# Optimization experiments

Hardware: AMD Instinct MI355X
Metric: run time of the kernel (lower is better)

The kernel has to match this reference:

```python
import jax, jax.numpy as jnp
import numpy as np

HEADS = 8  # from init_kwargs

def setup_inputs() -> dict:
    key = jax.random.key(0)
    ks = jax.random.split(key, 9)
    N, S, E = 8, 2048, 512
    scale = 1.0 / np.sqrt(E)
    return {
        "values": jax.random.normal(ks[0], (N, S, E), jnp.float32),
        "keys": jax.random.normal(ks[1], (N, S, E), jnp.float32),
        "query": jax.random.normal(ks[2], (N, S, E), jnp.float32),
        "mask": jnp.ones((N, 1, 1, S), jnp.int32),
        "Wv": jax.random.normal(ks[3], (E, E), jnp.float32) * scale,
        "Wk": jax.random.normal(ks[4], (E, E), jnp.float32) * scale,
        "Wq": jax.random.normal(ks[5], (E, E), jnp.float32) * scale,
        "Wo": jax.random.normal(ks[6], (E, E), jnp.float32) * scale,
        "bo": jnp.zeros((E,), jnp.float32),
    }

def reference(values, keys, query, mask, Wv, Wk, Wq, Wo, bo):
    N, Q, E = query.shape
    H = HEADS
    D = E // H
    v = (values @ Wv).reshape(N, -1, H, D)  # [N,K,H,D]
    k = (keys @ Wk).reshape(N, -1, H, D)
    q = (query @ Wq).reshape(N, Q, H, D)
    energy = jnp.einsum('nqhd,nkhd->nhqk', q, k)  # [N,H,Q,K]
    energy = jnp.where(mask == 0, jnp.float32(-1e20), energy)
    attn = jax.nn.softmax(energy / jnp.sqrt(jnp.float32(D)), axis=3)
    out = jnp.einsum('nhqk,nkhd->nqhd', attn, v).reshape(N, Q, E)
    return out @ Wo + bo
```

## Files before the change

### kernel.cpp

```cpp
#include <hip/hip_runtime.h>
#include <hip/hip_bf16.h>
#include <stdint.h>

typedef __bf16 bf16;
typedef __bf16 bf16x8 __attribute__((ext_vector_type(8)));
typedef __bf16 bf16x4v __attribute__((ext_vector_type(4)));
typedef float  f32x4  __attribute__((ext_vector_type(4)));
typedef float  f32x16 __attribute__((ext_vector_type(16)));
typedef unsigned int u32x4 __attribute__((ext_vector_type(4)));

#define NB    8
#define SEQ   2048
#define EMB   512
#define NHEAD 8
#define HD    64

static __device__ __forceinline__ f32x4 mfma16(bf16x8 a, bf16x8 b, f32x4 c) {
    return __builtin_amdgcn_mfma_f32_16x16x32_bf16(a, b, c, 0, 0, 0);
}
static __device__ __forceinline__ f32x16 mfma32(bf16x8 a, bf16x8 b, f32x16 c) {
    return __builtin_amdgcn_mfma_f32_32x32x16_bf16(a, b, c, 0, 0, 0);
}
static __device__ __forceinline__ float ex2(float x) {
    float r; asm("v_exp_f32 %0, %1" : "=v"(r) : "v"(x)); return r;
}
static __device__ __forceinline__ unsigned pkbf(float lo, float hi) {
    unsigned d; asm("v_cvt_pk_bf16_f32 %0, %1, %2" : "=v"(d) : "v"(lo), "v"(hi)); return d;
}
static __device__ __forceinline__ void gload_lds16(const void* g, void* l) {
    __builtin_amdgcn_global_load_lds(
        (const __attribute__((address_space(1))) unsigned int*)g,
        (__attribute__((address_space(3))) unsigned int*)l, 16, 0, 0);
}
static __device__ __forceinline__ int vposInv(int pos) {
    int p4  = pos >> 4;
    int r   = ((p4 & 1) << 3) | (pos & 7);
    int hi2 = (pos >> 3) & 1;
    return (p4 >> 1) * 32 + ((r & 3) | (hi2 << 2) | ((r >> 2) << 3));
}
#define PRIO1 __builtin_amdgcn_s_setprio(1)
#define PRIO0 __builtin_amdgcn_s_setprio(0)

__global__ __launch_bounds__(256) void prep_weights(
    const float* __restrict__ Wv, const float* __restrict__ Wk,
    const float* __restrict__ Wq, const float* __restrict__ Wo,
    bf16* __restrict__ wt)
{
    __shared__ float Ls[64][65];
    const int b    = blockIdx.x;
    const int wsel = b >> 6;
    const int kt   = (b & 63) >> 3;
    const int nt   = b & 7;
    const int t    = threadIdx.x;
    const float* src = (wsel == 0) ? Wv : (wsel == 1) ? Wk : (wsel == 2) ? Wq : Wo;

#pragma unroll
    for (int i = 0; i < 16; ++i) {
        int e = i * 256 + t;
        int k = e >> 6, n = e & 63;
        Ls[k][n] = src[(size_t)(kt * 64 + k) * 512 + nt * 64 + n];
    }
    __syncthreads();
#pragma unroll
    for (int i = 0; i < 16; ++i) {
        int e = i * 256 + t;
        int n = e >> 6, k = e & 63;
        wt[(size_t)wsel * 262144 + (size_t)(nt * 64 + n) * 512 + kt * 64 + k] = (bf16)Ls[k][n];
    }
}

__global__ __launch_bounds__(256) void proj_fused(
    const float* __restrict__ Av, const float* __restrict__ Ak,
    const float* __restrict__ Aq, const bf16* __restrict__ wt,
    bf16* __restrict__ VbP, bf16* __restrict__ Kb, bf16* __restrict__ Qb,
    float sc)
{
    __shared__ __align__(16) char smem[35328];
    bf16* As = (bf16*)smem;
    char* BsB = smem + 18432;

    const int t    = threadIdx.x;
    const int lane = t & 63;
    const int wave = t >> 6;
    const int wr   = wave >> 1, wc = wave & 1;
    const int l15  = lane & 15, lg = lane >> 4;
    const int z    = blockIdx.z;
    const long row0 = (long)blockIdx.x * 128;
    const int  col0 = blockIdx.y * 128;

    const float* A  = (z == 0) ? Av : (z == 1) ? Ak : Aq;
    const bf16*  Bt = wt + (size_t)z * 262144;
    const float  oscale = (z == 2) ? sc : 1.0f;

    f32x4 acc[4][4];
#pragma unroll
    for (int i = 0; i < 4; i++)
#pragma unroll
        for (int j = 0; j < 4; j++) acc[i][j] = (f32x4){0.f, 0.f, 0.f, 0.f};

    for (int k0 = 0; k0 < 512; k0 += 64) {
        __syncthreads();
#pragma unroll
        for (int i = 0; i < 8; i++) {
            int c  = t + 256 * i;
            int r  = c >> 4;
            int cc = (c & 15) * 4;
            f32x4 v = *(const f32x4*)(A + (row0 + r) * 512 + k0 + cc);
            bf16x4v pk = { (bf16)v[0], (bf16)v[1], (bf16)v[2], (bf16)v[3] };
            *(bf16x4v*)(As + r * 72 + cc) = pk;
        }
#pragma unroll
        for (int i = 0; i < 4; i++) {
            int chunk = i * 4 + wave;
            int c = chunk * 64 + lane;
            int r = c >> 3, u = c & 7;
            gload_lds16(Bt + (size_t)(col0 + r) * 512 + k0 + ((u ^ (r & 7)) << 3),
                        BsB + chunk * 1024);
        }
        __syncthreads();
#pragma unroll
        for (int kc = 0; kc < 64; kc += 32) {
            bf16x8 af[4], bfv[4];
#pragma unroll
            for (int mb = 0; mb < 4; mb++)
                af[mb] = *(bf16x8*)(As + (wr * 64 + mb * 16 + l15) * 72 + kc + lg * 8);
#pragma unroll
            for (int nb = 0; nb < 4; nb++) {
                int row = wc * 64 + nb * 16 + l15;
                bfv[nb] = *(bf16x8*)(BsB + row * 128 + (((lg + (kc >> 3)) ^ (l15 & 7)) << 4));
            }
#pragma unroll
            for (int mb = 0; mb < 4; mb++)
#pragma unroll
                for (int nb = 0; nb < 4; nb++)
                    acc[mb][nb] = mfma16(af[mb], bfv[nb], acc[mb][nb]);
        }
    }

    if (z == 0) {
        __syncthreads();
        bf16* Cs = (bf16*)smem;
#pragma unroll
        for (int mb = 0; mb < 4; mb++)
#pragma unroll
            for (int nb = 0; nb < 4; nb++)
#pragma unroll
                for (int r = 0; r < 4; r++) {
                    int keyl = wr * 64 + mb * 16 + lg * 4 + r;
                    int dl   = wc * 64 + nb * 16 + l15;
                    Cs[dl * 138 + keyl] = (bf16)acc[mb][nb][r];
                }
        __syncthreads();
        const int n_idx = (int)(row0 >> 11);
        const int key0  = (int)(row0 & 2047);
        const int dl    = t >> 1;
        const int half  = t & 1;
        const int x8    = (dl & 7) << 3;
        bf16* dst = VbP + ((size_t)n_idx * 512 + col0 + dl) * 2048 + key0 + half * 64;
#pragma unroll
        for (int cc = 0; cc < 8; ++cc) {
            bf16x8 v;
#pragma unroll
            for (int j = 0; j < 8; ++j)
                v[j] = Cs[dl * 138 + half * 64 + vposInv((cc * 8 + j) ^ x8)];
            *(bf16x8*)(dst + cc * 8) = v;
        }
    } else {
        bf16* Cp = (z == 1) ? Kb : Qb;
#pragma unroll
        for (int mb = 0; mb < 4; mb++)
#pragma unroll
            for (int nb = 0; nb < 4; nb++)
#pragma unroll
                for (int r = 0; r < 4; r++) {
                    long grow = row0 + wr * 64 + mb * 16 + lg * 4 + r;
                    int  gcol = col0 + wc * 64 + nb * 16 + l15;
                    Cp[grow * 512 + gcol] = (bf16)(acc[mb][nb][r] * oscale);
                }
    }
}

__global__ __launch_bounds__(256) void gemm_final(
    const bf16* __restrict__ Ap, const bf16* __restrict__ Bt,
    float* __restrict__ Cp, const float* __restrict__ bias)
{
    __shared__ __align__(16) char AsM[128 * 128];
    __shared__ __align__(16) bf16 Bs[128][64];

    const int t    = threadIdx.x;
    const int lane = t & 63;
    const int wave = t >> 6;
    const int wr   = wave >> 1, wc = wave & 1;
    const int l15  = lane & 15, lg = lane >> 4;
    const long row0 = (long)blockIdx.x * 128;
    const int  col0 = blockIdx.y * 128;

    f32x4 acc[4][4];
#pragma unroll
    for (int i = 0; i < 4; i++)
#pragma unroll
        for (int j = 0; j < 4; j++) acc[i][j] = (f32x4){0.f, 0.f, 0.f, 0.f};

    for (int k0 = 0; k0 < 512; k0 += 64) {
        __syncthreads();
#pragma unroll
        for (int i = 0; i < 4; i++) {
            int chunk = i * 4 + wave;
            int c = chunk * 64 + lane;
            int r = c >> 3, u = c & 7;
            gload_lds16(Ap + (row0 + r) * 512 + k0 + ((u ^ (r & 7)) << 3),
                        AsM + chunk * 1024);
        }
#pragma unroll
        for (int i = 0; i < 4; i++) {
            int chunk = i * 4 + wave;
            int c = chunk * 64 + lane;
            int r = c >> 3, u = c & 7;
            gload_lds16(Bt + (size_t)(col0 + r) * 512 + k0 + ((u ^ (r & 7)) << 3),
                        (char*)&Bs[0][0] + chunk * 1024);
        }
        __syncthreads();
#pragma unroll
        for (int kc = 0; kc < 64; kc += 32) {
            bf16x8 af[4], bfv[4];
#pragma unroll
            for (int mb = 0; mb < 4; mb++) {
                int row = wr * 64 + mb * 16 + l15;
                af[mb] = *(bf16x8*)(AsM + row * 128 + (((lg + (kc >> 3)) ^ (l15 & 7)) << 4));
            }
#pragma unroll
            for (int nb = 0; nb < 4; nb++) {
                int row = wc * 64 + nb * 16 + l15;
                bfv[nb] = *(bf16x8*)((char*)&Bs[0][0] + row * 128 + (((lg + (kc >> 3)) ^ (l15 & 7)) << 4));
            }
#pragma unroll
            for (int mb = 0; mb < 4; mb++)
#pragma unroll
                for (int nb = 0; nb < 4; nb++)
                    acc[mb][nb] = mfma16(af[mb], bfv[nb], acc[mb][nb]);
        }
    }

#pragma unroll
    for (int mb = 0; mb < 4; mb++)
#pragma unroll
        for (int nb = 0; nb < 4; nb++)
#pragma unroll
            for (int r = 0; r < 4; r++) {
                long grow = row0 + wr * 64 + mb * 16 + lg * 4 + r;
                int  gcol = col0 + wc * 64 + nb * 16 + l15;
                Cp[grow * 512 + gcol] = acc[mb][nb][r] + bias[gcol];
            }
}

__global__ __launch_bounds__(512, 2) void attn_kernel(
    const bf16* __restrict__ Qg, const bf16* __restrict__ Kg,
    const bf16* __restrict__ VbP, const int* __restrict__ mask,
    bf16* __restrict__ ctx)
{
    __shared__ __align__(16) bf16 Ks[4][4096];
    __shared__ __align__(16) bf16 Vt[4][4096];
    __shared__ __align__(16) bf16 Ob[8][32 * 72];

    const int t    = threadIdx.x;
    const int lane = t & 63;
    const int w    = t >> 6;
    const int l31  = lane & 31;
    const int hi   = lane >> 5;
    const int h = blockIdx.x, n = blockIdx.y, qt = blockIdx.z;

    const size_t nbase   = (size_t)n * SEQ;
    const size_t headoff = (size_t)h * 64;
    const int q0 = qt * 512 + w * 64;

    int* mflags = (int*)&Ob[0][0];
    {
        const int* mp0 = mask + n * SEQ + t * 4;
        int mok = (mp0[0] != 0) & (mp0[1] != 0) & (mp0[2] != 0) & (mp0[3] != 0);
        unsigned long long b = __ballot(mok);
        if (lane == 0) mflags[w] = (b == ~0ULL) ? 1 : 0;
    }

    bf16x8 qf[2][4];
#pragma unroll
    for (int qb = 0; qb < 2; ++qb)
#pragma unroll
        for (int ds = 0; ds < 4; ++ds)
            qf[qb][ds] = *(const bf16x8*)(Qg + (nbase + q0 + qb * 32 + l31) * 512 + headoff + ds * 16 + hi * 8);

    f32x16 o[2][2] = {};
    float l_run[2] = {0.f, 0.f};

    const bf16* kg = Kg + (nbase + w * 8 + (lane >> 3)) * 512 + headoff + (((lane & 7) ^ (lane >> 3)) << 3);
    const bf16* vgP = VbP + ((size_t)n * 512 + h * 64 + w * 8 + (lane >> 3)) * 2048 + ((lane & 7) << 3);
    const int*  mp = mask + n * SEQ;

    gload_lds16(kg,                    (char*)&Ks[0][0] + w * 1024);
    gload_lds16(kg + (size_t)64 * 512, (char*)&Ks[1][0] + w * 1024);
    gload_lds16(vgP,                   (char*)&Vt[0][0] + w * 1024);
    gload_lds16(vgP + 64,              (char*)&Vt[1][0] + w * 1024);
    __syncthreads();
    const int maskall = mflags[0] & mflags[1] & mflags[2] & mflags[3] &
                        mflags[4] & mflags[5] & mflags[6] & mflags[7];

    f32x16 p[2][2];
    u32x4  bq[2][4];

#define QK_TILE(KB) do {                                                      \
        const char* kbb = (const char*)(KB);                                  \
        f32x16 zz = {};                                                       \
        p[0][0] = zz; p[0][1] = zz; p[1][0] = zz; p[1][1] = zz;               \
        PRIO1;                                                                \
        _Pragma("unroll")                                                     \
        for (int ds = 0; ds < 4; ++ds) {                                      \
            int sw = (ds * 32 + hi * 16) ^ ((l31 & 7) << 4);                  \
            bf16x8 kf0 = *(const bf16x8*)(kbb + l31 * 128 + sw);              \
            bf16x8 kf1 = *(const bf16x8*)(kbb + (32 + l31) * 128 + sw);       \
            p[0][0] = mfma32(kf0, qf[0][ds], p[0][0]);                        \
            p[1][0] = mfma32(kf0, qf[1][ds], p[1][0]);                        \
            p[0][1] = mfma32(kf1, qf[0][ds], p[0][1]);                        \
            p[1][1] = mfma32(kf1, qf[1][ds], p[1][1]);                        \
        }                                                                     \
        PRIO0;                                                                \
    } while (0)

#define MASK_TILE(T) do {                                                     \
        if (!maskall) {                                                       \
            int mv = mp[(T) * 64 + lane];                                     \
            unsigned long long mb = __ballot(mv != 0);                        \
            if (mb != ~0ULL) {                                                \
                _Pragma("unroll") for (int qb = 0; qb < 2; ++qb)              \
                _Pragma("unroll") for (int kb = 0; kb < 2; ++kb) {            \
                    float* pp = (float*)&p[qb][kb];                           \
                    _Pragma("unroll") for (int r = 0; r < 16; ++r) {          \
                        int kk = kb * 32 + (r & 3) + 8 * (r >> 2) + 4 * hi;   \
                        if (!((mb >> kk) & 1)) pp[r] = -1e30f;                \
                    }                                                         \
                }                                                             \
            }                                                                 \
        }                                                                     \
    } while (0)

#define SM_PACK do {                                                          \
        _Pragma("unroll")                                                     \
        for (int qb = 0; qb < 2; ++qb) {                                      \
            float* p0 = (float*)&p[qb][0];                                    \
            float* p1 = (float*)&p[qb][1];                                    \
            float sa0 = 0.f, sa1 = 0.f, sa2 = 0.f, sa3 = 0.f;                 \
            _Pragma("unroll") for (int r = 0; r < 16; r += 4) {               \
                float e0 = ex2(p0[r]);   p0[r]   = e0; sa0 += e0;             \
                float e1 = ex2(p0[r+1]); p0[r+1] = e1; sa1 += e1;             \
                float e2 = ex2(p0[r+2]); p0[r+2] = e2; sa2 += e2;             \
                float e3 = ex2(p0[r+3]); p0[r+3] = e3; sa3 += e3;             \
            }                                                                 \
            _Pragma("unroll") for (int r = 0; r < 16; r += 4) {               \
                float e0 = ex2(p1[r]);   p1[r]   = e0; sa0 += e0;             \
                float e1 = ex2(p1[r+1]); p1[r+1] = e1; sa1 += e1;             \
                float e2 = ex2(p1[r+2]); p1[r+2] = e2; sa2 += e2;             \
                float e3 = ex2(p1[r+3]); p1[r+3] = e3; sa3 += e3;             \
            }                                                                 \
            float sl = (sa0 + sa1) + (sa2 + sa3);                             \
            l_run[qb] += sl + __shfl_xor(sl, 32);                             \
            _Pragma("unroll")                                                 \
            for (int ks = 0; ks < 4; ++ks) {                                  \
                float* ps = (ks >> 1) ? p1 : p0;                              \
                int bo = (ks & 1) * 8;                                        \
                bq[qb][ks] = (u32x4){ pkbf(ps[bo + 0], ps[bo + 1]),           \
                                      pkbf(ps[bo + 2], ps[bo + 3]),           \
                                      pkbf(ps[bo + 4], ps[bo + 5]),           \
                                      pkbf(ps[bo + 6], ps[bo + 7]) };         \
            }                                                                 \
        }                                                                     \
    } while (0)

#define PV_TILE(VB) do {                                                      \
        const char* vbb = (const char*)(VB);                                  \
        PRIO1;                                                                \
        _Pragma("unroll")                                                     \
        for (int ks = 0; ks < 4; ++ks) {                                      \
            int sw = (ks * 32 + hi * 16) ^ ((l31 & 7) << 4);                  \
            bf16x8 vf0 = *(const bf16x8*)(vbb + l31 * 128 + sw);              \
            bf16x8 vf1 = *(const bf16x8*)(vbb + (32 + l31) * 128 + sw);       \
            union { u32x4 u; bf16x8 v; } c0, c1;                              \
            c0.u = bq[0][ks]; c1.u = bq[1][ks];                               \
            o[0][0] = mfma32(vf0, c0.v, o[0][0]);                             \
            o[0][1] = mfma32(vf0, c1.v, o[0][1]);                             \
            o[1][0] = mfma32(vf1, c0.v, o[1][0]);                             \
            o[1][1] = mfma32(vf1, c1.v, o[1][1]);                             \
        }                                                                     \
        PRIO0;                                                                \
    } while (0)

    for (int e = 0; e < 16; ++e) {
        const int bA = (e & 1) * 2, bB = bA + 1;
        const int nA = bA ^ 2,      nB = bB ^ 2;
        if (e < 15) {
            gload_lds16(kg + (size_t)(2 * e + 2) * 64 * 512, (char*)&Ks[nA][0] + w * 1024);
            gload_lds16(kg + (size_t)(2 * e + 3) * 64 * 512, (char*)&Ks[nB][0] + w * 1024);
            gload_lds16(vgP + (2 * e + 2) * 64,              (char*)&Vt[nA][0] + w * 1024);
            gload_lds16(vgP + (2 * e + 3) * 64,              (char*)&Vt[nB][0] + w * 1024);
        }
        QK_TILE(&Ks[bA][0]);
        MASK_TILE(2 * e);
        SM_PACK;
        PV_TILE(&Vt[bA][0]);
        QK_TILE(&Ks[bB][0]);
        MASK_TILE(2 * e + 1);
        SM_PACK;
        PV_TILE(&Vt[bB][0]);
        __syncthreads();
    }

#pragma unroll
    for (int qb = 0; qb < 2; ++qb) {
        float inv = 1.f / l_run[qb];
        bf16* ob = &Ob[w][0];
#pragma unroll
        for (int db = 0; db < 2; ++db) {
            float* oo = (float*)&o[db][qb];
#pragma unroll
            for (int r = 0; r < 16; ++r) {
                int d = db * 32 + (r & 3) + 8 * (r >> 2) + 4 * hi;
                ob[l31 * 72 + d] = (bf16)(oo[r] * inv);
            }
        }
#pragma unroll
        for (int i = 0; i < 2; ++i)
#pragma unroll
            for (int half = 0; half < 2; ++half) {
                int ql = i * 16 + (lane >> 2);
                int d8 = (lane & 3) * 8 + half * 32;
                bf16x8 vv = *(const bf16x8*)(ob + ql * 72 + d8);
                *(bf16x8*)(ctx + (nbase + q0 + qb * 32 + ql) * 512 + headoff + d8) = vv;
            }
    }
#undef QK_TILE
#undef MASK_TILE
#undef SM_PACK
#undef PV_TILE
}

extern "C" void kernel_launch(void* const* d_in, const int* in_sizes, int n_in,
                              void* d_out, int out_size, void* d_ws, size_t ws_size,
                              hipStream_t stream) {
    (void)in_sizes; (void)n_in; (void)out_size; (void)ws_size;
    const float* values = (const float*)d_in[0];
    const float* keys   = (const float*)d_in[1];
    const float* query  = (const float*)d_in[2];
    const int*   mask   = (const int*)d_in[3];
    const float* Wv = (const float*)d_in[4];
    const float* Wk = (const float*)d_in[5];
    const float* Wq = (const float*)d_in[6];
    const float* Wo = (const float*)d_in[7];
    const float* bo = (const float*)d_in[8];
    float* out = (float*)d_out;

    char* ws = (char*)d_ws;
    bf16* wt  = (bf16*)(ws);
    bf16* Qb  = (bf16*)(ws + ((size_t)2  << 20));
    bf16* Kb  = (bf16*)(ws + ((size_t)18 << 20));
    bf16* VbP = (bf16*)(ws + ((size_t)34 << 20));
    bf16* Cb  = (bf16*)(ws + ((size_t)50 << 20));

    const float SC = 0.18033688011f;

    prep_weights<<<256, 256, 0, stream>>>(Wv, Wk, Wq, Wo, wt);
    proj_fused<<<dim3(128, 4, 3), 256, 0, stream>>>(values, keys, query, wt,
                                                    VbP, Kb, Qb, SC);
    attn_kernel<<<dim3(8, 8, 4), 512, 0, stream>>>(Qb, Kb, VbP, mask, Cb);
    gemm_final<<<dim3(128, 4), 256, 0, stream>>>(Cb, wt + 3 * 262144, out, bo);
}
```

Baseline: 156.1 us.

## Retile projection and output GEMMs to full-width 64x512 blocks with 8 waves

Both the QKV projection and the output projection GEMMs now use 64-row by full-512-column tiles with 512 threads, each wave owning a 64-column slice. The A tile (fp32 activations) is loaded and converted once per row block instead of once per column block, so the redundant re-reads of activations across four column tiles go away. The cost is a larger LDS footprint (about 73 KB), fewer blocks, and re-reading the whole weight matrix per row block. The V transpose epilogue is reworked to a per-wave staging buffer.

```diff
diff --git a/kernel.cpp b/kernel.cpp
--- a/kernel.cpp
+++ b/kernel.cpp
@@ -69,24 +69,21 @@
     }
 }
 
-__global__ __launch_bounds__(256) void proj_fused(
+__global__ __launch_bounds__(512, 2) void proj_fused(
     const float* __restrict__ Av, const float* __restrict__ Ak,
     const float* __restrict__ Aq, const bf16* __restrict__ wt,
     bf16* __restrict__ VbP, bf16* __restrict__ Kb, bf16* __restrict__ Qb,
     float sc)
 {
-    __shared__ __align__(16) char smem[35328];
-    bf16* As = (bf16*)smem;
-    char* BsB = smem + 18432;
+    __shared__ __align__(16) char smem[74752];
+    bf16* As = (bf16*)(smem + 65536);
 
     const int t    = threadIdx.x;
     const int lane = t & 63;
-    const int wave = t >> 6;
-    const int wr   = wave >> 1, wc = wave & 1;
+    const int w    = t >> 6;
     const int l15  = lane & 15, lg = lane >> 4;
     const int z    = blockIdx.z;
-    const long row0 = (long)blockIdx.x * 128;
-    const int  col0 = blockIdx.y * 128;
+    const long row0 = (long)blockIdx.x * 64;
 
     const float* A  = (z == 0) ? Av : (z == 1) ? Ak : Aq;
     const bf16*  Bt = wt + (size_t)z * 262144;
@@ -98,24 +95,24 @@
 #pragma unroll
         for (int j = 0; j < 4; j++) acc[i][j] = (f32x4){0.f, 0.f, 0.f, 0.f};
 
+    const int ar  = t >> 3;
+    const int acc8 = (t & 7) * 8;
+
     for (int k0 = 0; k0 < 512; k0 += 64) {
         __syncthreads();
+        {
+            f32x4 v0 = *(const f32x4*)(A + (row0 + ar) * 512 + k0 + acc8);
+            f32x4 v1 = *(const f32x4*)(A + (row0 + ar) * 512 + k0 + acc8 + 4);
+            bf16x8 pk = { (bf16)v0[0], (bf16)v0[1], (bf16)v0[2], (bf16)v0[3],
+                          (bf16)v1[0], (bf16)v1[1], (bf16)v1[2], (bf16)v1[3] };
+            *(bf16x8*)(As + ar * 72 + acc8) = pk;
+        }
 #pragma unroll
         for (int i = 0; i < 8; i++) {
-            int c  = t + 256 * i;
-            int r  = c >> 4;
-            int cc = (c & 15) * 4;
-            f32x4 v = *(const f32x4*)(A + (row0 + r) * 512 + k0 + cc);
-            bf16x4v pk = { (bf16)v[0], (bf16)v[1], (bf16)v[2], (bf16)v[3] };
-            *(bf16x4v*)(As + r * 72 + cc) = pk;
-        }
-#pragma unroll
-        for (int i = 0; i < 4; i++) {
-            int chunk = i * 4 + wave;
-            int c = chunk * 64 + lane;
-            int r = c >> 3, u = c & 7;
-            gload_lds16(Bt + (size_t)(col0 + r) * 512 + k0 + ((u ^ (r & 7)) << 3),
-                        BsB + chunk * 1024);
+            int chunk = w * 8 + i;
+            int r = chunk * 8 + (lane >> 3), u = lane & 7;
+            gload_lds16(Bt + (size_t)r * 512 + k0 + ((u ^ (r & 7)) << 3),
+                        smem + chunk * 1024);
         }
         __syncthreads();
 #pragma unroll
@@ -123,11 +120,11 @@
             bf16x8 af[4], bfv[4];
 #pragma unroll
             for (int mb = 0; mb < 4; mb++)
-                af[mb] = *(bf16x8*)(As + (wr * 64 + mb * 16 + l15) * 72 + kc + lg * 8);
+                af[mb] = *(bf16x8*)(As + (mb * 16 + l15) * 72 + kc + lg * 8);
 #pragma unroll
             for (int nb = 0; nb < 4; nb++) {
-                int row = wc * 64 + nb * 16 + l15;
-                bfv[nb] = *(bf16x8*)(BsB + row * 128 + (((lg + (kc >> 3)) ^ (l15 & 7)) << 4));
+                int row = w * 64 + nb * 16 + l15;
+                bfv[nb] = *(bf16x8*)(smem + row * 128 + (((lg + (kc >> 3)) ^ (l15 & 7)) << 4));
             }
 #pragma unroll
             for (int mb = 0; mb < 4; mb++)
@@ -139,30 +136,29 @@
 
     if (z == 0) {
         __syncthreads();
-        bf16* Cs = (bf16*)smem;
+        bf16* csw = (bf16*)smem + w * 4608;
 #pragma unroll
         for (int mb = 0; mb < 4; mb++)
 #pragma unroll
             for (int nb = 0; nb < 4; nb++)
 #pragma unroll
                 for (int r = 0; r < 4; r++) {
-                    int keyl = wr * 64 + mb * 16 + lg * 4 + r;
-                    int dl   = wc * 64 + nb * 16 + l15;
-                    Cs[dl * 138 + keyl] = (bf16)acc[mb][nb][r];
+                    int keyl = mb * 16 + lg * 4 + r;
+                    int dl   = nb * 16 + l15;
+                    csw[dl * 72 + keyl] = (bf16)acc[mb][nb][r];
                 }
         __syncthreads();
         const int n_idx = (int)(row0 >> 11);
         const int key0  = (int)(row0 & 2047);
-        const int dl    = t >> 1;
-        const int half  = t & 1;
-        const int x8    = (dl & 7) << 3;
-        bf16* dst = VbP + ((size_t)n_idx * 512 + col0 + dl) * 2048 + key0 + half * 64;
+        const int d     = w * 64 + lane;
+        const int x8    = (lane & 7) << 3;
+        bf16* dst = VbP + ((size_t)n_idx * 512 + d) * 2048 + key0;
 #pragma unroll
         for (int cc = 0; cc < 8; ++cc) {
             bf16x8 v;
 #pragma unroll
             for (int j = 0; j < 8; ++j)
-                v[j] = Cs[dl * 138 + half * 64 + vposInv((cc * 8 + j) ^ x8)];
+                v[j] = csw[lane * 72 + vposInv((cc * 8 + j) ^ x8)];
             *(bf16x8*)(dst + cc * 8) = v;
         }
     } else {
@@ -173,27 +169,25 @@
             for (int nb = 0; nb < 4; nb++)
 #pragma unroll
                 for (int r = 0; r < 4; r++) {
-                    long grow = row0 + wr * 64 + mb * 16 + lg * 4 + r;
-                    int  gcol = col0 + wc * 64 + nb * 16 + l15;
+                    long grow = row0 + mb * 16 + lg * 4 + r;
+                    int  gcol = w * 64 + nb * 16 + l15;
                     Cp[grow * 512 + gcol] = (bf16)(acc[mb][nb][r] * oscale);
                 }
     }
 }
 
-__global__ __launch_bounds__(256) void gemm_final(
+__global__ __launch_bounds__(512, 2) void gemm_final(
     const bf16* __restrict__ Ap, const bf16* __restrict__ Bt,
     float* __restrict__ Cp, const float* __restrict__ bias)
 {
-    __shared__ __align__(16) char AsM[128 * 128];
-    __shared__ __align__(16) bf16 Bs[128][64];
+    __shared__ __align__(16) char smem[73728];
+    char* AsB = smem + 65536;
 
     const int t    = threadIdx.x;
     const int lane = t & 63;
-    const int wave = t >> 6;
-    const int wr   = wave >> 1, wc = wave & 1;
+    const int w    = t >> 6;
     const int l15  = lane & 15, lg = lane >> 4;
-    const long row0 = (long)blockIdx.x * 128;
-    const int  col0 = blockIdx.y * 128;
+    const long row0 = (long)blockIdx.x * 64;
 
     f32x4 acc[4][4];
 #pragma unroll
@@ -203,21 +197,17 @@
 
     for (int k0 = 0; k0 < 512; k0 += 64) {
         __syncthreads();
-#pragma unroll
-        for (int i = 0; i < 4; i++) {
-            int chunk = i * 4 + wave;
-            int c = chunk * 64 + lane;
-            int r = c >> 3, u = c & 7;
+        {
+            int r = w * 8 + (lane >> 3), u = lane & 7;
             gload_lds16(Ap + (row0 + r) * 512 + k0 + ((u ^ (r & 7)) << 3),
-                        AsM + chunk * 1024);
-        }
-#pragma unroll
-        for (int i = 0; i < 4; i++) {
-            int chunk = i * 4 + wave;
-            int c = chunk * 64 + lane;
-            int r = c >> 3, u = c & 7;
-            gload_lds16(Bt + (size_t)(col0 + r) * 512 + k0 + ((u ^ (r & 7)) << 3),
-                        (char*)&Bs[0][0] + chunk * 1024);
+                        AsB + w * 1024);
+        }
+#pragma unroll
+        for (int i = 0; i < 8; i++) {
+            int chunk = w * 8 + i;
+            int r = chunk * 8 + (lane >> 3), u = lane & 7;
+            gload_lds16(Bt + (size_t)r * 512 + k0 + ((u ^ (r & 7)) << 3),
+                        smem + chunk * 1024);
         }
         __syncthreads();
 #pragma unroll
@@ -225,13 +215,13 @@
             bf16x8 af[4], bfv[4];
 #pragma unroll
             for (int mb = 0; mb < 4; mb++) {
-                int row = wr * 64 + mb * 16 + l15;
-                af[mb] = *(bf16x8*)(AsM + row * 128 + (((lg + (kc >> 3)) ^ (l15 & 7)) << 4));
+                int row = mb * 16 + l15;
+                af[mb] = *(bf16x8*)(AsB + row * 128 + (((lg + (kc >> 3)) ^ (l15 & 7)) << 4));
             }
 #pragma unroll
             for (int nb = 0; nb < 4; nb++) {
-                int row = wc * 64 + nb * 16 + l15;
-                bfv[nb] = *(bf16x8*)((char*)&Bs[0][0] + row * 128 + (((lg + (kc >> 3)) ^ (l15 & 7)) << 4));
+                int row = w * 64 + nb * 16 + l15;
+                bfv[nb] = *(bf16x8*)(smem + row * 128 + (((lg + (kc >> 3)) ^ (l15 & 7)) << 4));
             }
 #pragma unroll
             for (int mb = 0; mb < 4; mb++)
@@ -247,8 +237,8 @@
         for (int nb = 0; nb < 4; nb++)
 #pragma unroll
             for (int r = 0; r < 4; r++) {
-                long grow = row0 + wr * 64 + mb * 16 + lg * 4 + r;
-                int  gcol = col0 + wc * 64 + nb * 16 + l15;
+                long grow = row0 + mb * 16 + lg * 4 + r;
+                int  gcol = w * 64 + nb * 16 + l15;
                 Cp[grow * 512 + gcol] = acc[mb][nb][r] + bias[gcol];
             }
 }
@@ -465,8 +455,8 @@
     const float SC = 0.18033688011f;
 
     prep_weights<<<256, 256, 0, stream>>>(Wv, Wk, Wq, Wo, wt);
-    proj_fused<<<dim3(128, 4, 3), 256, 0, stream>>>(values, keys, query, wt,
+    proj_fused<<<dim3(256, 1, 3), 512, 0, stream>>>(values, keys, query, wt,
                                                     VbP, Kb, Qb, SC);
     attn_kernel<<<dim3(8, 8, 4), 512, 0, stream>>>(Qb, Kb, VbP, mask, Cb);
-    gemm_final<<<dim3(128, 4), 256, 0, stream>>>(Cb, wt + 3 * 262144, out, bo);
-}
+    gemm_final<<<256, 512, 0, stream>>>(Cb, wt + 3 * 262144, out, bo);
+}
```

After: 159.0 us. No clear change (+1.9%).

## Halve per-wave query rows and double attention grid, unify LDS buffer

Applied to the files above, without the earlier changes.

Each wave now processes 32 query rows instead of 64, so a block covers 256 queries and the grid doubles to 512 blocks. This raises parallelism across CUs and cuts register pressure (fewer accumulators). LDS is merged into one 64KB buffer that is reused for the output staging. The trade-off is that each K/V tile loaded into LDS feeds half as many MFMAs, so global and LDS traffic per FLOP doubles.

```diff
diff --git a/kernel.cpp b/kernel.cpp
--- a/kernel.cpp
+++ b/kernel.cpp
@@ -258,9 +258,7 @@
     const bf16* __restrict__ VbP, const int* __restrict__ mask,
     bf16* __restrict__ ctx)
 {
-    __shared__ __align__(16) bf16 Ks[4][4096];
-    __shared__ __align__(16) bf16 Vt[4][4096];
-    __shared__ __align__(16) bf16 Ob[8][32 * 72];
+    __shared__ __align__(16) char smem[65536];
 
     const int t    = threadIdx.x;
     const int lane = t & 63;
@@ -271,55 +269,53 @@
 
     const size_t nbase   = (size_t)n * SEQ;
     const size_t headoff = (size_t)h * 64;
-    const int q0 = qt * 512 + w * 64;
-
-    int* mflags = (int*)&Ob[0][0];
+    const int q0 = qt * 256 + w * 32;
+
     {
         const int* mp0 = mask + n * SEQ + t * 4;
         int mok = (mp0[0] != 0) & (mp0[1] != 0) & (mp0[2] != 0) & (mp0[3] != 0);
         unsigned long long b = __ballot(mok);
-        if (lane == 0) mflags[w] = (b == ~0ULL) ? 1 : 0;
-    }
-
-    bf16x8 qf[2][4];
-#pragma unroll
-    for (int qb = 0; qb < 2; ++qb)
-#pragma unroll
-        for (int ds = 0; ds < 4; ++ds)
-            qf[qb][ds] = *(const bf16x8*)(Qg + (nbase + q0 + qb * 32 + l31) * 512 + headoff + ds * 16 + hi * 8);
-
-    f32x16 o[2][2] = {};
-    float l_run[2] = {0.f, 0.f};
+        if (lane == 0) ((int*)smem)[w] = (b == ~0ULL) ? 1 : 0;
+    }
+    __syncthreads();
+    int maskall = 1;
+#pragma unroll
+    for (int i = 0; i < 8; ++i) maskall &= ((int*)smem)[i];
+    __syncthreads();
+
+    bf16x8 qf[4];
+#pragma unroll
+    for (int ds = 0; ds < 4; ++ds)
+        qf[ds] = *(const bf16x8*)(Qg + (nbase + q0 + l31) * 512 + headoff + ds * 16 + hi * 8);
+
+    f32x16 o[2] = {};
+    float l_run = 0.f;
 
     const bf16* kg = Kg + (nbase + w * 8 + (lane >> 3)) * 512 + headoff + (((lane & 7) ^ (lane >> 3)) << 3);
     const bf16* vgP = VbP + ((size_t)n * 512 + h * 64 + w * 8 + (lane >> 3)) * 2048 + ((lane & 7) << 3);
     const int*  mp = mask + n * SEQ;
 
-    gload_lds16(kg,                    (char*)&Ks[0][0] + w * 1024);
-    gload_lds16(kg + (size_t)64 * 512, (char*)&Ks[1][0] + w * 1024);
-    gload_lds16(vgP,                   (char*)&Vt[0][0] + w * 1024);
-    gload_lds16(vgP + 64,              (char*)&Vt[1][0] + w * 1024);
+    gload_lds16(kg,                    smem + 0 * 8192 + w * 1024);
+    gload_lds16(kg + (size_t)64 * 512, smem + 1 * 8192 + w * 1024);
+    gload_lds16(vgP,                   smem + 32768 + 0 * 8192 + w * 1024);
+    gload_lds16(vgP + 64,              smem + 32768 + 1 * 8192 + w * 1024);
     __syncthreads();
-    const int maskall = mflags[0] & mflags[1] & mflags[2] & mflags[3] &
-                        mflags[4] & mflags[5] & mflags[6] & mflags[7];
-
-    f32x16 p[2][2];
-    u32x4  bq[2][4];
-
-#define QK_TILE(KB) do {                                                      \
-        const char* kbb = (const char*)(KB);                                  \
+
+    f32x16 p[2];
+    u32x4  bq[4];
+
+#define QK_TILE(BUF) do {                                                     \
+        const char* kbb = smem + (BUF) * 8192;                                \
         f32x16 zz = {};                                                       \
-        p[0][0] = zz; p[0][1] = zz; p[1][0] = zz; p[1][1] = zz;               \
+        p[0] = zz; p[1] = zz;                                                 \
         PRIO1;                                                                \
         _Pragma("unroll")                                                     \
         for (int ds = 0; ds < 4; ++ds) {                                      \
             int sw = (ds * 32 + hi * 16) ^ ((l31 & 7) << 4);                  \
             bf16x8 kf0 = *(const bf16x8*)(kbb + l31 * 128 + sw);              \
             bf16x8 kf1 = *(const bf16x8*)(kbb + (32 + l31) * 128 + sw);       \
-            p[0][0] = mfma32(kf0, qf[0][ds], p[0][0]);                        \
-            p[1][0] = mfma32(kf0, qf[1][ds], p[1][0]);                        \
-            p[0][1] = mfma32(kf1, qf[0][ds], p[0][1]);                        \
-            p[1][1] = mfma32(kf1, qf[1][ds], p[1][1]);                        \
+            p[0] = mfma32(kf0, qf[ds], p[0]);                                 \
+            p[1] = mfma32(kf1, qf[ds], p[1]);                                 \
         }                                                                     \
         PRIO0;                                                                \
     } while (0)
@@ -329,9 +325,8 @@
             int mv = mp[(T) * 64 + lane];                                     \
             unsigned long long mb = __ballot(mv != 0);                        \
             if (mb != ~0ULL) {                                                \
-                _Pragma("unroll") for (int qb = 0; qb < 2; ++qb)              \
                 _Pragma("unroll") for (int kb = 0; kb < 2; ++kb) {            \
-                    float* pp = (float*)&p[qb][kb];                           \
+                    float* pp = (float*)&p[kb];                               \
                     _Pragma("unroll") for (int r = 0; r < 16; ++r) {          \
                         int kk = kb * 32 + (r & 3) + 8 * (r >> 2) + 4 * hi;   \
                         if (!((mb >> kk) & 1)) pp[r] = -1e30f;                \
@@ -342,51 +337,46 @@
     } while (0)
 
 #define SM_PACK do {                                                          \
+        float* p0 = (float*)&p[0];                                            \
+        float* p1 = (float*)&p[1];                                            \
+        float sa0 = 0.f, sa1 = 0.f, sa2 = 0.f, sa3 = 0.f;                     \
+        _Pragma("unroll") for (int r = 0; r < 16; r += 4) {                   \
+            float e0 = ex2(p0[r]);   p0[r]   = e0; sa0 += e0;                 \
+            float e1 = ex2(p0[r+1]); p0[r+1] = e1; sa1 += e1;                 \
+            float e2 = ex2(p0[r+2]); p0[r+2] = e2; sa2 += e2;                 \
+            float e3 = ex2(p0[r+3]); p0[r+3] = e3; sa3 += e3;                 \
+        }                                                                     \
+        _Pragma("unroll") for (int r = 0; r < 16; r += 4) {                   \
+            float e0 = ex2(p1[r]);   p1[r]   = e0; sa0 += e0;                 \
+            float e1 = ex2(p1[r+1]); p1[r+1] = e1; sa1 += e1;                 \
+            float e2 = ex2(p1[r+2]); p1[r+2] = e2; sa2 += e2;                 \
+            float e3 = ex2(p1[r+3]); p1[r+3] = e3; sa3 += e3;                 \
+        }                                                                     \
+        float sl = (sa0 + sa1) + (sa2 + sa3);                                 \
+        l_run += sl + __shfl_xor(sl, 32);                                     \
         _Pragma("unroll")                                                     \
-        for (int qb = 0; qb < 2; ++qb) {                                      \
-            float* p0 = (float*)&p[qb][0];                                    \
-            float* p1 = (float*)&p[qb][1];                                    \
-            float sa0 = 0.f, sa1 = 0.f, sa2 = 0.f, sa3 = 0.f;                 \
-            _Pragma("unroll") for (int r = 0; r < 16; r += 4) {               \
-                float e0 = ex2(p0[r]);   p0[r]   = e0; sa0 += e0;             \
-                float e1 = ex2(p0[r+1]); p0[r+1] = e1; sa1 += e1;             \
-                float e2 = ex2(p0[r+2]); p0[r+2] = e2; sa2 += e2;             \
-                float e3 = ex2(p0[r+3]); p0[r+3] = e3; sa3 += e3;             \
-            }                                                                 \
-            _Pragma("unroll") for (int r = 0; r < 16; r += 4) {               \
-                float e0 = ex2(p1[r]);   p1[r]   = e0; sa0 += e0;             \
-                float e1 = ex2(p1[r+1]); p1[r+1] = e1; sa1 += e1;             \
-                float e2 = ex2(p1[r+2]); p1[r+2] = e2; sa2 += e2;             \
-                float e3 = ex2(p1[r+3]); p1[r+3] = e3; sa3 += e3;             \
-            }                                                                 \
-            float sl = (sa0 + sa1) + (sa2 + sa3);                             \
-            l_run[qb] += sl + __shfl_xor(sl, 32);                             \
-            _Pragma("unroll")                                                 \
-            for (int ks = 0; ks < 4; ++ks) {                                  \
-                float* ps = (ks >> 1) ? p1 : p0;                              \
-                int bo = (ks & 1) * 8;                                        \
-                bq[qb][ks] = (u32x4){ pkbf(ps[bo + 0], ps[bo + 1]),           \
-                                      pkbf(ps[bo + 2], ps[bo + 3]),           \
-                                      pkbf(ps[bo + 4], ps[bo + 5]),           \
-                                      pkbf(ps[bo + 6], ps[bo + 7]) };         \
-            }                                                                 \
+        for (int ks = 0; ks < 4; ++ks) {                                      \
+            float* ps = (ks >> 1) ? p1 : p0;                                  \
+            int bo = (ks & 1) * 8;                                            \
+            bq[ks] = (u32x4){ pkbf(ps[bo + 0], ps[bo + 1]),                   \
+                              pkbf(ps[bo + 2], ps[bo + 3]),                   \
+                              pkbf(ps[bo + 4], ps[bo + 5]),                   \
+                              pkbf(ps[bo + 6], ps[bo + 7]) };                 \
         }                                                                     \
     } while (0)
 
-#define PV_TILE(VB) do {                                                      \
-        const char* vbb = (const char*)(VB);                                  \
+#define PV_TILE(BUF) do {                                                     \
+        const char* vbb = smem + 32768 + (BUF) * 8192;                        \
         PRIO1;                                                                \
         _Pragma("unroll")                                                     \
         for (int ks = 0; ks < 4; ++ks) {                                      \
             int sw = (ks * 32 + hi * 16) ^ ((l31 & 7) << 4);                  \
             bf16x8 vf0 = *(const bf16x8*)(vbb + l31 * 128 + sw);              \
             bf16x8 vf1 = *(const bf16x8*)(vbb + (32 + l31) * 128 + sw);       \
-            union { u32x4 u; bf16x8 v; } c0, c1;                              \
-            c0.u = bq[0][ks]; c1.u = bq[1][ks];                               \
-            o[0][0] = mfma32(vf0, c0.v, o[0][0]);                             \
-            o[0][1] = mfma32(vf0, c1.v, o[0][1]);                             \
-            o[1][0] = mfma32(vf1, c0.v, o[1][0]);                             \
-            o[1][1] = mfma32(vf1, c1.v, o[1][1]);                             \
+            union { u32x4 u; bf16x8 v; } c0;                                  \
+            c0.u = bq[ks];                                                    \
+            o[0] = mfma32(vf0, c0.v, o[0]);                                   \
+            o[1] = mfma32(vf1, c0.v, o[1]);                                   \
         }                                                                     \
         PRIO0;                                                                \
     } while (0)
@@ -395,35 +385,35 @@
         const int bA = (e & 1) * 2, bB = bA + 1;
         const int nA = bA ^ 2,      nB = bB ^ 2;
         if (e < 15) {
-            gload_lds16(kg + (size_t)(2 * e + 2) * 64 * 512, (char*)&Ks[nA][0] + w * 1024);
-            gload_lds16(kg + (size_t)(2 * e + 3) * 64 * 512, (char*)&Ks[nB][0] + w * 1024);
-            gload_lds16(vgP + (2 * e + 2) * 64,              (char*)&Vt[nA][0] + w * 1024);
-            gload_lds16(vgP + (2 * e + 3) * 64,              (char*)&Vt[nB][0] + w * 1024);
-        }
-        QK_TILE(&Ks[bA][0]);
+            gload_lds16(kg + (size_t)(2 * e + 2) * 64 * 512, smem + nA * 8192 + w * 1024);
+            gload_lds16(kg + (size_t)(2 * e + 3) * 64 * 512, smem + nB * 8192 + w * 1024);
+            gload_lds16(vgP + (2 * e + 2) * 64, smem + 32768 + nA * 8192 + w * 1024);
+            gload_lds16(vgP + (2 * e + 3) * 64, smem + 32768 + nB * 8192 + w * 1024);
+        }
+        QK_TILE(bA);
         MASK_TILE(2 * e);
         SM_PACK;
-        PV_TILE(&Vt[bA][0]);
-        QK_TILE(&Ks[bB][0]);
+        PV_TILE(bA);
+        QK_TILE(bB);
         MASK_TILE(2 * e + 1);
         SM_PACK;
-        PV_TILE(&Vt[bB][0]);
-        __syncthreads();
-    }
-
-#pragma unroll
-    for (int qb = 0; qb < 2; ++qb) {
-        float inv = 1.f / l_run[qb];
-        bf16* ob = &Ob[w][0];
+        PV_TILE(bB);
+        __syncthreads();
+    }
+
+    {
+        float inv = 1.f / l_run;
+        bf16* ob = (bf16*)(smem + w * 4608);
 #pragma unroll
         for (int db = 0; db < 2; ++db) {
-            float* oo = (float*)&o[db][qb];
+            float* oo = (float*)&o[db];
 #pragma unroll
             for (int r = 0; r < 16; ++r) {
                 int d = db * 32 + (r & 3) + 8 * (r >> 2) + 4 * hi;
                 ob[l31 * 72 + d] = (bf16)(oo[r] * inv);
             }
         }
+        __syncthreads();
 #pragma unroll
         for (int i = 0; i < 2; ++i)
 #pragma unroll
@@ -431,7 +421,7 @@
                 int ql = i * 16 + (lane >> 2);
                 int d8 = (lane & 3) * 8 + half * 32;
                 bf16x8 vv = *(const bf16x8*)(ob + ql * 72 + d8);
-                *(bf16x8*)(ctx + (nbase + q0 + qb * 32 + ql) * 512 + headoff + d8) = vv;
+                *(bf16x8*)(ctx + (nbase + q0 + ql) * 512 + headoff + d8) = vv;
             }
     }
 #undef QK_TILE
@@ -467,6 +457,6 @@
     prep_weights<<<256, 256, 0, stream>>>(Wv, Wk, Wq, Wo, wt);
     proj_fused<<<dim3(128, 4, 3), 256, 0, stream>>>(values, keys, query, wt,
                                                     VbP, Kb, Qb, SC);
-    attn_kernel<<<dim3(8, 8, 4), 512, 0, stream>>>(Qb, Kb, VbP, mask, Cb);
+    attn_kernel<<<dim3(8, 8, 8), 512, 0, stream>>>(Qb, Kb, VbP, mask, Cb);
     gemm_final<<<dim3(128, 4), 256, 0, stream>>>(Cb, wt + 3 * 262144, out, bo);
 }
```

Result: no change. 154.2 us (-1.2%).

## Alias attention LDS buffers into one pool and interleave QK with PV

Applied to the files above, without the earlier changes.

The separate K, V, output and mask-flag shared arrays are replaced by a single 64 KB byte pool. The output staging area and mask flags now reuse the K region, with extra barriers added around the mask-flag reduction. The goal is to cut LDS per block so that two 512-thread blocks can be resident per CU, as the launch bounds request. The second tile's QK matmul is also moved ahead of the first tile's PV matmul, giving the scheduler independent MFMA work to overlap with the softmax. The cost is two added barriers and higher register pressure from holding p and bq live together.

```diff
diff --git a/kernel.cpp b/kernel.cpp
--- a/kernel.cpp
+++ b/kernel.cpp
@@ -258,9 +258,7 @@
     const bf16* __restrict__ VbP, const int* __restrict__ mask,
     bf16* __restrict__ ctx)
 {
-    __shared__ __align__(16) bf16 Ks[4][4096];
-    __shared__ __align__(16) bf16 Vt[4][4096];
-    __shared__ __align__(16) bf16 Ob[8][32 * 72];
+    __shared__ __align__(16) char smem[65536];
 
     const int t    = threadIdx.x;
     const int lane = t & 63;
@@ -273,13 +271,17 @@
     const size_t headoff = (size_t)h * 64;
     const int q0 = qt * 512 + w * 64;
 
-    int* mflags = (int*)&Ob[0][0];
     {
         const int* mp0 = mask + n * SEQ + t * 4;
         int mok = (mp0[0] != 0) & (mp0[1] != 0) & (mp0[2] != 0) & (mp0[3] != 0);
         unsigned long long b = __ballot(mok);
-        if (lane == 0) mflags[w] = (b == ~0ULL) ? 1 : 0;
-    }
+        if (lane == 0) ((int*)smem)[w] = (b == ~0ULL) ? 1 : 0;
+    }
+    __syncthreads();
+    int maskall = 1;
+#pragma unroll
+    for (int i = 0; i < 8; ++i) maskall &= ((int*)smem)[i];
+    __syncthreads();
 
     bf16x8 qf[2][4];
 #pragma unroll
@@ -295,19 +297,17 @@
     const bf16* vgP = VbP + ((size_t)n * 512 + h * 64 + w * 8 + (lane >> 3)) * 2048 + ((lane & 7) << 3);
     const int*  mp = mask + n * SEQ;
 
-    gload_lds16(kg,                    (char*)&Ks[0][0] + w * 1024);
-    gload_lds16(kg + (size_t)64 * 512, (char*)&Ks[1][0] + w * 1024);
-    gload_lds16(vgP,                   (char*)&Vt[0][0] + w * 1024);
-    gload_lds16(vgP + 64,              (char*)&Vt[1][0] + w * 1024);
+    gload_lds16(kg,                    smem + 0 * 8192 + w * 1024);
+    gload_lds16(kg + (size_t)64 * 512, smem + 1 * 8192 + w * 1024);
+    gload_lds16(vgP,                   smem + 32768 + 0 * 8192 + w * 1024);
+    gload_lds16(vgP + 64,              smem + 32768 + 1 * 8192 + w * 1024);
     __syncthreads();
-    const int maskall = mflags[0] & mflags[1] & mflags[2] & mflags[3] &
-                        mflags[4] & mflags[5] & mflags[6] & mflags[7];
 
     f32x16 p[2][2];
     u32x4  bq[2][4];
 
-#define QK_TILE(KB) do {                                                      \
-        const char* kbb = (const char*)(KB);                                  \
+#define QK_TILE(BUF) do {                                                     \
+        const char* kbb = smem + (BUF) * 8192;                                \
         f32x16 zz = {};                                                       \
         p[0][0] = zz; p[0][1] = zz; p[1][0] = zz; p[1][1] = zz;               \
         PRIO1;                                                                \
@@ -373,8 +373,8 @@
         }                                                                     \
     } while (0)
 
-#define PV_TILE(VB) do {                                                      \
-        const char* vbb = (const char*)(VB);                                  \
+#define PV_TILE(BUF) do {                                                     \
+        const char* vbb = smem + 32768 + (BUF) * 8192;                        \
         PRIO1;                                                                \
         _Pragma("unroll")                                                     \
         for (int ks = 0; ks < 4; ++ks) {                                      \
@@ -395,26 +395,26 @@
         const int bA = (e & 1) * 2, bB = bA + 1;
         const int nA = bA ^ 2,      nB = bB ^ 2;
         if (e < 15) {
-            gload_lds16(kg + (size_t)(2 * e + 2) * 64 * 512, (char*)&Ks[nA][0] + w * 1024);
-            gload_lds16(kg + (size_t)(2 * e + 3) * 64 * 512, (char*)&Ks[nB][0] + w * 1024);
-            gload_lds16(vgP + (2 * e + 2) * 64,              (char*)&Vt[nA][0] + w * 1024);
-            gload_lds16(vgP + (2 * e + 3) * 64,              (char*)&Vt[nB][0] + w * 1024);
-        }
-        QK_TILE(&Ks[bA][0]);
+            gload_lds16(kg + (size_t)(2 * e + 2) * 64 * 512, smem + nA * 8192 + w * 1024);
+            gload_lds16(kg + (size_t)(2 * e + 3) * 64 * 512, smem + nB * 8192 + w * 1024);
+            gload_lds16(vgP + (2 * e + 2) * 64, smem + 32768 + nA * 8192 + w * 1024);
+            gload_lds16(vgP + (2 * e + 3) * 64, smem + 32768 + nB * 8192 + w * 1024);
+        }
+        QK_TILE(bA);
         MASK_TILE(2 * e);
         SM_PACK;
-        PV_TILE(&Vt[bA][0]);
-        QK_TILE(&Ks[bB][0]);
+        QK_TILE(bB);
+        PV_TILE(bA);
         MASK_TILE(2 * e + 1);
         SM_PACK;
-        PV_TILE(&Vt[bB][0]);
+        PV_TILE(bB);
         __syncthreads();
     }
 
 #pragma unroll
     for (int qb = 0; qb < 2; ++qb) {
         float inv = 1.f / l_run[qb];
-        bf16* ob = &Ob[w][0];
+        bf16* ob = (bf16*)(smem + w * 4608);
 #pragma unroll
         for (int db = 0; db < 2; ++db) {
             float* oo = (float*)&o[db][qb];
```

After: 159.3 us. +2.0%, slower.
